# Kernel tuning notes

Measured on AMD Instinct MI355X. Metric: run time of the kernel, lower is better.

The kernel has to match this reference:

```python
import jax, jax.numpy as jnp
import numpy as np

D_MODEL = 384
N_HEADS = 8
HEAD_DIM = D_MODEL // N_HEADS


def setup_inputs() -> dict:
    key = jax.random.key(0)
    ks = jax.random.split(key, 8)
    b, n = 2, 2048
    s = 0.02
    return {
        "x": jax.random.normal(ks[0], (b, n, D_MODEL), jnp.float32),
        "coords": jax.random.normal(ks[1], (b, n, 3), jnp.float32),
        "W_qkv": jax.random.normal(ks[2], (D_MODEL, 3 * D_MODEL), jnp.float32) * s,
        "b_qkv": jnp.zeros((3 * D_MODEL,), jnp.float32),
        "W_dist": jax.random.normal(ks[3], (1, N_HEADS), jnp.float32) * s,
        "b_dist": jnp.zeros((N_HEADS,), jnp.float32),
        "W_out": jax.random.normal(ks[4], (D_MODEL, D_MODEL), jnp.float32) * s,
        "b_out": jnp.zeros((D_MODEL,), jnp.float32),
    }


def reference(x, coords, W_qkv, b_qkv, W_dist, b_dist, W_out, b_out):
    b, n, _ = x.shape
    qkv = x @ W_qkv + b_qkv                       # (b, n, 3*d)
    q, k, v = jnp.split(qkv, 3, axis=-1)
    def heads(t):
        return t.reshape(b, n, N_HEADS, HEAD_DIM).transpose(0, 2, 1, 3)  # b h n d
    q, k, v = heads(q), heads(k), heads(v)
    attn = jnp.einsum('bhid,bhjd->bhij', q, k) / jnp.sqrt(jnp.float32(HEAD_DIM))
    # distance bias: ||c_i - c_j|| projected to heads (Linear(1, n_heads))
    diff = coords[:, :, None, :] - coords[:, None, :, :]   # (b, i, j, 3)
    dist = jnp.sqrt(jnp.sum(diff * diff, axis=-1))         # (b, i, j)
    dist_bias = dist[..., None] * W_dist[0] + b_dist       # (b, i, j, h)
    attn = attn + dist_bias.transpose(0, 3, 1, 2)          # (b, h, i, j)
    attn = jax.nn.softmax(attn, axis=-1)
    out = jnp.einsum('bhij,bhjd->bhid', attn, v)
    out = out.transpose(0, 2, 1, 3).reshape(b, n, D_MODEL)
    return out @ W_out + b_out
```

## Files before the change

### kernel.cpp

```cpp
#include <hip/hip_runtime.h>
#include <hip/hip_bf16.h>

#define NB 2
#define SEQ 2048
#define DM 384
#define NH 8
#define HD 48
#define QKVN 1152

typedef __hip_bfloat16 bf16;
typedef __attribute__((ext_vector_type(8))) short short8;
typedef __attribute__((ext_vector_type(4))) float float4v;
typedef __attribute__((ext_vector_type(16))) float f32x16;

static __device__ __forceinline__ float bf2f(bf16 v){ return __bfloat162float(v); }
static __device__ __forceinline__ float ldin(const void* p, size_t i, int isf){
    return isf ? ((const float*)p)[i] : bf2f(((const bf16*)p)[i]);
}
static __device__ __forceinline__ short f2b(float f){
    union { float f; unsigned u; } a; a.f = f;
    unsigned r = a.u + 0x7FFFu + ((a.u >> 16) & 1u);
    return (short)(r >> 16);
}
static __device__ __forceinline__ unsigned pk2(float a, float b){
    union { __hip_bfloat162 h; unsigned u; } r;
    r.h = __float22bfloat162_rn(float2{a, b});
    return r.u;
}
static __device__ __forceinline__ float bflo(unsigned u){
    union { unsigned u; float f; } a; a.u = u << 16; return a.f;
}
static __device__ __forceinline__ float bfhi(unsigned u){
    union { unsigned u; float f; } a; a.u = u & 0xFFFF0000u; return a.f;
}
static __device__ __forceinline__ short8 u4pack(unsigned w0, unsigned w1, unsigned w2, unsigned w3){
    union { unsigned u[4]; short8 s; } r; r.u[0]=w0; r.u[1]=w1; r.u[2]=w2; r.u[3]=w3; return r.s;
}
static __device__ __forceinline__ int detect_isf(const void* x){
    const unsigned short* xb = (const unsigned short*)x;
    int l = threadIdx.x & 63;
    union { unsigned u; float f; } a; a.u = ((unsigned)xb[2*l]) << 16;
    float ab = fabsf(a.f);
    int good = (a.f == 0.0f) || (ab > 9.765625e-4f && ab < 1024.0f);
    unsigned long long m = __ballot(good);
    return (__popcll(m) >= 32) ? 0 : 1;
}

__global__ __launch_bounds__(256) void k_wt(const void* __restrict__ x,
    const void* __restrict__ Wqkv, short* __restrict__ WqT)
{
    const int isf = detect_isf(x);
    const int t = threadIdx.x;
    const int b = blockIdx.x;
    const int kt = b / 36, nt = b % 36;
    const int k0 = kt*32, n0 = nt*32;
    __shared__ float Ls[32][33];
    for (int idx = t; idx < 1024; idx += 256) {
        int r = idx >> 5, c = idx & 31;
        Ls[r][c] = ldin(Wqkv, (size_t)(k0+r)*QKVN + n0 + c, isf);
    }
    __syncthreads();
    for (int idx = t; idx < 1024; idx += 256) {
        int r2 = idx >> 5, c2 = idx & 31;
        WqT[(size_t)(n0+r2)*DM + k0 + c2] = f2b(Ls[c2][r2]);
    }
}

__global__ __launch_bounds__(256) void k_qkv_dist(const void* __restrict__ x,
    const void* __restrict__ coords,
    const short* __restrict__ WT, const void* __restrict__ bqkv,
    const void* __restrict__ Wout,
    short* __restrict__ qg3, short* __restrict__ kg3, short* __restrict__ vg3,
    short* __restrict__ dist8, short* __restrict__ WoT)
{
    __shared__ __align__(16) short As[64*72];
    __shared__ __align__(16) short Bs[128*72];
    __shared__ float cjx[16], cjy[16], cjz[16];
    const int isf = detect_isf(x);
    const int t = threadIdx.x;
    const int bid = blockIdx.x;
    if (bid >= 1088) {
        const int b = bid - 1088;
        const int kt = b / 12, nt = b % 12;
        const int k0 = kt*32, n0 = nt*32;
        float (*Ls)[33] = (float(*)[33])As;
        for (int idx = t; idx < 1024; idx += 256) {
            int r = idx >> 5, c = idx & 31;
            Ls[r][c] = ldin(Wout, (size_t)(k0+r)*DM + n0 + c, isf);
        }
        __syncthreads();
        for (int idx = t; idx < 1024; idx += 256) {
            int r2 = idx >> 5, c2 = idx & 31;
            WoT[(size_t)(n0+r2)*DM + k0 + c2] = f2b(Ls[c2][r2]);
        }
        return;
    }
    if (bid >= 576) {
        const int b = bid - 576;
        const int bb = b >> 8;
        const int jg = (b >> 1) & 127;
        const int j0 = jg * 16;
        const int ih = (b & 1) * 1024;
        if (t < 16) {
            int gj = (bb*SEQ + j0 + t)*3;
            cjx[t] = ldin(coords, gj, isf);
            cjy[t] = ldin(coords, gj+1, isf);
            cjz[t] = ldin(coords, gj+2, isf);
        }
        __syncthreads();
        #pragma unroll
        for (int k = 0; k < 4; ++k) {
            int i = ih + k*256 + t;
            int gi = (bb*SEQ + i)*3;
            float px = ldin(coords, gi, isf), py = ldin(coords, gi+1, isf), pz = ldin(coords, gi+2, isf);
            short o[16];
            #pragma unroll
            for (int e = 0; e < 16; ++e) {
                float dx = px - cjx[e], dy = py - cjy[e], dz = pz - cjz[e];
                o[e] = f2b(sqrtf(dx*dx + dy*dy + dz*dz));
            }
            short* dst = dist8 + (((size_t)bb*512 + (size_t)jg*4)*SEQ + i)*4;
            *(int2*)(dst)          = *(const int2*)(o);
            *(int2*)(dst + SEQ*4)  = *(const int2*)(o + 4);
            *(int2*)(dst + SEQ*8)  = *(const int2*)(o + 8);
            *(int2*)(dst + SEQ*12) = *(const int2*)(o + 12);
        }
        return;
    }
    const int w = t >> 6, lane = t & 63, L = lane & 15, quad = lane >> 4;
    const int mt = bid / 9, nt = bid % 9;
    const int row0 = mt*64, col0 = nt*128;
    const int wm = w & 1, wn = w >> 1;
    float4v acc[2][4] = {};
    int4 rA[4], rB[4];
    {
        const int k0 = 0;
        #pragma unroll
        for (int ci = 0; ci < 2; ++ci) {
            int c = t + ci*256; int row = c >> 3, k8 = c & 7;
            size_t src = (size_t)(row0+row)*DM + k0 + k8*8;
            if (isf) {
                rA[2*ci]   = *(const int4*)((const float*)x + src);
                rA[2*ci+1] = *(const int4*)((const float*)x + src + 4);
            } else {
                rA[ci] = *(const int4*)((const short*)x + src);
            }
        }
        #pragma unroll
        for (int ci = 0; ci < 4; ++ci) {
            int c = t + ci*256; int row = c >> 3, k8 = c & 7;
            rB[ci] = *(const int4*)(WT + (size_t)(col0+row)*DM + k0 + k8*8);
        }
    }
    for (int ks = 0; ks < 6; ++ks) {
        __syncthreads();
        #pragma unroll
        for (int ci = 0; ci < 2; ++ci) {
            int c = t + ci*256; int row = c >> 3, k8 = c & 7;
            if (isf) {
                union { int4 i[2]; float f[8]; } u; u.i[0] = rA[2*ci]; u.i[1] = rA[2*ci+1];
                short o[8];
                #pragma unroll
                for (int e = 0; e < 8; ++e) o[e] = f2b(u.f[e]);
                *(int4*)(&As[row*72 + k8*8]) = *(const int4*)o;
            } else {
                *(int4*)(&As[row*72 + k8*8]) = rA[ci];
            }
        }
        #pragma unroll
        for (int ci = 0; ci < 4; ++ci) {
            int c = t + ci*256; int row = c >> 3, k8 = c & 7;
            *(int4*)(&Bs[row*72 + k8*8]) = rB[ci];
        }
        __syncthreads();
        if (ks < 5) {
            const int k0 = (ks+1)*64;
            #pragma unroll
            for (int ci = 0; ci < 2; ++ci) {
                int c = t + ci*256; int row = c >> 3, k8 = c & 7;
                size_t src = (size_t)(row0+row)*DM + k0 + k8*8;
                if (isf) {
                    rA[2*ci]   = *(const int4*)((const float*)x + src);
                    rA[2*ci+1] = *(const int4*)((const float*)x + src + 4);
                } else {
                    rA[ci] = *(const int4*)((const short*)x + src);
                }
            }
            #pragma unroll
            for (int ci = 0; ci < 4; ++ci) {
                int c = t + ci*256; int row = c >> 3, k8 = c & 7;
                rB[ci] = *(const int4*)(WT + (size_t)(col0+row)*DM + k0 + k8*8);
            }
        }
        #pragma unroll
        for (int kc = 0; kc < 2; ++kc) {
            short8 a0 = *(const short8*)(&As[(32*wm + L)*72 + kc*32 + quad*8]);
            short8 a1 = *(const short8*)(&As[(32*wm + 16 + L)*72 + kc*32 + quad*8]);
            #pragma unroll
            for (int ni = 0; ni < 4; ++ni) {
                short8 bf = *(const short8*)(&Bs[(64*wn + 16*ni + L)*72 + kc*32 + quad*8]);
                acc[0][ni] = __builtin_amdgcn_mfma_f32_16x16x32_bf16(a0, bf, acc[0][ni], 0, 0, 0);
                acc[1][ni] = __builtin_amdgcn_mfma_f32_16x16x32_bf16(a1, bf, acc[1][ni], 0, 0, 0);
            }
        }
    }
    const int which = col0 / DM;
    const int cbase = col0 % DM;
    short* Ep = Bs;
    __syncthreads();
    if (which < 2) {
        #pragma unroll
        for (int mi = 0; mi < 2; ++mi)
            #pragma unroll
            for (int ni = 0; ni < 4; ++ni) {
                int col_l = 64*wn + 16*ni + L;
                float bv = ldin(bqkv, col0 + col_l, isf);
                #pragma unroll
                for (int r = 0; r < 4; ++r) {
                    int row_l = 32*wm + 16*mi + quad*4 + r;
                    Ep[row_l*136 + col_l] = f2b(acc[mi][ni][r] + bv);
                }
            }
        __syncthreads();
        short* dst = which ? kg3 : qg3;
        for (int c = t; c < 1024; c += 256) {
            int row_l = c >> 4, col_l = (c & 15)*8;
            int row_g = row0 + row_l;
            int bi = row_g >> 11, nn = row_g & (SEQ-1);
            int c2 = cbase + col_l;
            int hh = c2/HD, dh = c2%HD;
            int bh = bi*NH + hh;
            int dc = dh >> 4, hi = (dh >> 3) & 1;
            size_t dstoff = ((size_t)bh*64 + (nn>>5))*1536 + (size_t)((dc*2 + hi)*256 + (nn&31)*8);
            *(int4*)(dst + dstoff) = *(const int4*)(&Ep[row_l*136 + col_l]);
        }
    } else {
        #pragma unroll
        for (int mi = 0; mi < 2; ++mi)
            #pragma unroll
            for (int ni = 0; ni < 4; ++ni) {
                int col_l = 64*wn + 16*ni + L;
                float bv = ldin(bqkv, col0 + col_l, isf);
                #pragma unroll
                for (int r = 0; r < 4; ++r) {
                    int row_l = 32*wm + 16*mi + quad*4 + r;
                    Ep[col_l*72 + row_l] = f2b(acc[mi][ni][r] + bv);
                }
            }
        __syncthreads();
        for (int c = t; c < 1024; c += 256) {
            int col_l = c >> 3, row8 = (c & 7)*8;
            int row_g = row0 + row8;
            int bi = row_g >> 11, nn = row_g & (SEQ-1);
            int c2 = cbase + col_l;
            int hh = c2/HD, dh = c2%HD;
            int bh = bi*NH + hh;
            int jt = nn >> 5, jc = (nn >> 4) & 1;
            int ehalf = ((nn >> 3) & 1)*4;
            int dt = dh >> 5, dp = dh & 31;
            int hstride = dt ? 128 : 256;
            size_t base = ((size_t)bh*64 + jt)*1536 + (size_t)(jc*768 + dt*512 + dp*8 + ehalf);
            *(int2*)(vg3 + base)           = *(const int2*)(&Ep[col_l*72 + row8]);
            *(int2*)(vg3 + base + hstride) = *(const int2*)(&Ep[col_l*72 + row8 + 4]);
        }
    }
}

__global__ __launch_bounds__(256, 4) void k_attn(
    const short* __restrict__ qg3, const short* __restrict__ kg3, const short* __restrict__ vg3,
    const short* __restrict__ dist8, const void* __restrict__ Wdist,
    const void* __restrict__ bdist, short* __restrict__ aob, const void* __restrict__ x)
{
    __shared__ float Ored[2][32*48];
    __shared__ float Lred[2][32];
    const int isf = detect_isf(x);
    const int t = threadIdx.x;
    const int w = t >> 6, lane = t & 63;
    const int li = lane & 31, hi = lane >> 5;
    const int xcd  = blockIdx.x & 7;
    const int slot = blockIdx.x >> 3;
    const int bi   = xcd >> 2;
    const int band = xcd & 3;
    const int hh   = slot & 7;
    const int it   = band*16 + (slot >> 3);
    const int bh   = bi*NH + hh;
    const int i0 = it*32;
    const float log2e = 1.4426950408889634f;
    const float scale2 = 0.14433756729740643f * log2e;
    const float wd = ldin(Wdist, hh, isf) * log2e;
    const float bd = ldin(bdist, hh, isf) * log2e;

    const short* qB = qg3 + ((size_t)bh*64 + it)*1536 + hi*256 + li*8;
    const short8 qf0 = *(const short8*)(qB);
    const short8 qf1 = *(const short8*)(qB + 512);
    const short8 qf2 = *(const short8*)(qB + 1024);

    f32x16 accO0 = {}, accO1 = {};
    float rsum = 0.0f;

    const short* kBp = kg3 + ((size_t)bh*64 + w)*1536 + hi*256 + li*8;
    const short* vBp = vg3 + ((size_t)bh*64 + w)*1536 + li*8;
    const short* dBp = dist8 + (((size_t)bi*512 + (size_t)w*8 + hi)*SEQ + i0 + li)*4;

    for (int s = 0; s < 16; ++s) {
        short8 kf0 = *(const short8*)(kBp);
        short8 kf1 = *(const short8*)(kBp + 512);
        short8 kf2 = *(const short8*)(kBp + 1024);
        int2 du0 = *(const int2*)(dBp);
        int2 du1 = *(const int2*)(dBp + SEQ*8);
        int2 du2 = *(const int2*)(dBp + SEQ*16);
        int2 du3 = *(const int2*)(dBp + SEQ*24);
        f32x16 sacc = {};
        __builtin_amdgcn_s_setprio(1);
        sacc = __builtin_amdgcn_mfma_f32_32x32x16_bf16(kf0, qf0, sacc, 0, 0, 0);
        sacc = __builtin_amdgcn_mfma_f32_32x32x16_bf16(kf1, qf1, sacc, 0, 0, 0);
        sacc = __builtin_amdgcn_mfma_f32_32x32x16_bf16(kf2, qf2, sacc, 0, 0, 0);
        __builtin_amdgcn_s_setprio(0);
        float p[16];
        #pragma unroll
        for (int rq = 0; rq < 4; ++rq) {
            int2 du = rq == 0 ? du0 : rq == 1 ? du1 : rq == 2 ? du2 : du3;
            float d0 = bflo((unsigned)du.x), d1 = bfhi((unsigned)du.x);
            float d2 = bflo((unsigned)du.y), d3 = bfhi((unsigned)du.y);
            p[4*rq+0] = __builtin_amdgcn_exp2f(fmaf(sacc[4*rq+0], scale2, fmaf(d0, wd, bd)));
            p[4*rq+1] = __builtin_amdgcn_exp2f(fmaf(sacc[4*rq+1], scale2, fmaf(d1, wd, bd)));
            p[4*rq+2] = __builtin_amdgcn_exp2f(fmaf(sacc[4*rq+2], scale2, fmaf(d2, wd, bd)));
            p[4*rq+3] = __builtin_amdgcn_exp2f(fmaf(sacc[4*rq+3], scale2, fmaf(d3, wd, bd)));
            rsum += (p[4*rq+0] + p[4*rq+1]) + (p[4*rq+2] + p[4*rq+3]);
        }
        short8 pa0 = u4pack(pk2(p[0],p[1]),  pk2(p[2],p[3]),  pk2(p[4],p[5]),   pk2(p[6],p[7]));
        short8 pa1 = u4pack(pk2(p[8],p[9]),  pk2(p[10],p[11]),pk2(p[12],p[13]), pk2(p[14],p[15]));
        short8 v00 = *(const short8*)(vBp + hi*256);
        short8 v10 = *(const short8*)(vBp + 768 + hi*256);
        short8 v01 = *(const short8*)(vBp + 512 + hi*128);
        short8 v11 = *(const short8*)(vBp + 1280 + hi*128);
        __builtin_amdgcn_s_setprio(1);
        accO0 = __builtin_amdgcn_mfma_f32_32x32x16_bf16(pa0, v00, accO0, 0, 0, 0);
        accO0 = __builtin_amdgcn_mfma_f32_32x32x16_bf16(pa1, v10, accO0, 0, 0, 0);
        accO1 = __builtin_amdgcn_mfma_f32_32x32x16_bf16(pa0, v01, accO1, 0, 0, 0);
        accO1 = __builtin_amdgcn_mfma_f32_32x32x16_bf16(pa1, v11, accO1, 0, 0, 0);
        __builtin_amdgcn_s_setprio(0);
        kBp += 4*1536; vBp += 4*1536; dBp += (size_t)SEQ*128;
    }
    rsum += __shfl_xor(rsum, 32);

    if (w >= 2) {
        float* Od = Ored[w-2];
        #pragma unroll
        for (int r = 0; r < 16; ++r) {
            int ii = (r & 3) + 8*(r >> 2) + 4*hi;
            Od[ii*48 + li] = accO0[r];
            if (li < 16) Od[ii*48 + 32 + li] = accO1[r];
        }
        if (lane < 32) Lred[w-2][lane] = rsum;
    }
    __syncthreads();
    if (w < 2) {
        const float* Od = Ored[w];
        #pragma unroll
        for (int r = 0; r < 16; ++r) {
            int ii = (r & 3) + 8*(r >> 2) + 4*hi;
            accO0[r] += Od[ii*48 + li];
            accO1[r] += Od[ii*48 + 32 + (li & 15)];
        }
        rsum += Lred[w][li];
    }
    __syncthreads();
    if (w == 1) {
        float* Od = Ored[0];
        #pragma unroll
        for (int r = 0; r < 16; ++r) {
            int ii = (r & 3) + 8*(r >> 2) + 4*hi;
            Od[ii*48 + li] = accO0[r];
            if (li < 16) Od[ii*48 + 32 + li] = accO1[r];
        }
        if (lane < 32) Lred[0][lane] = rsum;
    }
    __syncthreads();
    if (w == 0) {
        float* Od = Ored[0];
        #pragma unroll
        for (int r = 0; r < 16; ++r) {
            int ii = (r & 3) + 8*(r >> 2) + 4*hi;
            Od[ii*48 + li] += accO0[r];
            if (li < 16) Od[ii*48 + 32 + li] += accO1[r];
        }
        if (lane < 32) Lred[0][lane] += rsum;
    }
    __syncthreads();
    for (int c = t; c < 192; c += 256) {
        int r = c / 6, d8 = (c % 6)*8;
        float inv = 1.0f / Lred[0][r];
        const float* src = &Ored[0][r*48 + d8];
        short o[8];
        #pragma unroll
        for (int e = 0; e < 8; ++e) o[e] = f2b(src[e]*inv);
        *(int4*)(aob + ((size_t)(bi*SEQ) + i0 + r)*DM + hh*HD + d8) = *(const int4*)o;
    }
}

__global__ __launch_bounds__(256) void k_out(const short* __restrict__ aob,
    const short* __restrict__ WT, const void* __restrict__ bout,
    void* __restrict__ out, const void* __restrict__ x)
{
    __shared__ __align__(16) short As[64*72];
    __shared__ __align__(16) short Bs[128*72];
    const int isf = detect_isf(x);
    const int t = threadIdx.x;
    const int w = t >> 6, lane = t & 63, L = lane & 15, quad = lane >> 4;
    const int mt = blockIdx.x / 3, nt = blockIdx.x % 3;
    const int row0 = mt*64, col0 = nt*128;
    const int wm = w & 1, wn = w >> 1;
    float4v acc[2][4] = {};
    int4 rA[2], rB[4];
    {
        #pragma unroll
        for (int ci = 0; ci < 2; ++ci) {
            int c = t + ci*256; int row = c >> 3, k8 = c & 7;
            rA[ci] = *(const int4*)(aob + (size_t)(row0+row)*DM + k8*8);
        }
        #pragma unroll
        for (int ci = 0; ci < 4; ++ci) {
            int c = t + ci*256; int row = c >> 3, k8 = c & 7;
            rB[ci] = *(const int4*)(WT + (size_t)(col0+row)*DM + k8*8);
        }
    }
    for (int ks = 0; ks < 6; ++ks) {
        __syncthreads();
        #pragma unroll
        for (int ci = 0; ci < 2; ++ci) {
            int c = t + ci*256; int row = c >> 3, k8 = c & 7;
            *(int4*)(&As[row*72 + k8*8]) = rA[ci];
        }
        #pragma unroll
        for (int ci = 0; ci < 4; ++ci) {
            int c = t + ci*256; int row = c >> 3, k8 = c & 7;
            *(int4*)(&Bs[row*72 + k8*8]) = rB[ci];
        }
        __syncthreads();
        if (ks < 5) {
            const int k0 = (ks+1)*64;
            #pragma unroll
            for (int ci = 0; ci < 2; ++ci) {
                int c = t + ci*256; int row = c >> 3, k8 = c & 7;
                rA[ci] = *(const int4*)(aob + (size_t)(row0+row)*DM + k0 + k8*8);
            }
            #pragma unroll
            for (int ci = 0; ci < 4; ++ci) {
                int c = t + ci*256; int row = c >> 3, k8 = c & 7;
                rB[ci] = *(const int4*)(WT + (size_t)(col0+row)*DM + k0 + k8*8);
            }
        }
        #pragma unroll
        for (int kc = 0; kc < 2; ++kc) {
            short8 a0 = *(const short8*)(&As[(32*wm + L)*72 + kc*32 + quad*8]);
            short8 a1 = *(const short8*)(&As[(32*wm + 16 + L)*72 + kc*32 + quad*8]);
            #pragma unroll
            for (int ni = 0; ni < 4; ++ni) {
                short8 bf = *(const short8*)(&Bs[(64*wn + 16*ni + L)*72 + kc*32 + quad*8]);
                acc[0][ni] = __builtin_amdgcn_mfma_f32_16x16x32_bf16(a0, bf, acc[0][ni], 0, 0, 0);
                acc[1][ni] = __builtin_amdgcn_mfma_f32_16x16x32_bf16(a1, bf, acc[1][ni], 0, 0, 0);
            }
        }
    }
    #pragma unroll
    for (int mi = 0; mi < 2; ++mi) {
        #pragma unroll
        for (int ni = 0; ni < 4; ++ni) {
            int col_g = col0 + 64*wn + 16*ni + L;
            float bv = ldin(bout, col_g, isf);
            #pragma unroll
            for (int r = 0; r < 4; ++r) {
                int row_g = row0 + 32*wm + 16*mi + quad*4 + r;
                size_t oi = (size_t)row_g*DM + col_g;
                float val = acc[mi][ni][r] + bv;
                if (isf) ((float*)out)[oi] = val;
                else     ((bf16*)out)[oi]  = __float2bfloat16(val);
            }
        }
    }
}

extern "C" void kernel_launch(void* const* d_in, const int* in_sizes, int n_in,
                              void* d_out, int out_size, void* d_ws, size_t ws_size,
                              hipStream_t stream) {
    const void* x      = d_in[0];
    const void* coords = d_in[1];
    const void* Wqkv   = d_in[2];
    const void* bqkv   = d_in[3];
    const void* Wdist  = d_in[4];
    const void* bdist  = d_in[5];
    const void* Wout   = d_in[6];
    const void* bout   = d_in[7];

    short* qg3   = (short*)d_ws;
    short* kg3   = qg3  + (size_t)1572864;
    short* vg3   = kg3  + (size_t)1572864;
    short* dist8 = vg3  + (size_t)1573120;
    short* aob   = dist8 + (size_t)8388608;
    short* WqT   = aob  + (size_t)1572864;
    short* WoT   = WqT  + (size_t)442368;

    k_wt<<<dim3(432), dim3(256), 0, stream>>>(x, Wqkv, WqT);
    k_qkv_dist<<<dim3(1232), dim3(256), 0, stream>>>(x, coords, WqT, bqkv, Wout,
                                                     qg3, kg3, vg3, dist8, WoT);
    k_attn<<<dim3(1024), dim3(256), 0, stream>>>(qg3, kg3, vg3, dist8, Wdist, bdist, aob, x);
    k_out<<<dim3(192), dim3(256), 0, stream>>>(aob, WoT, bout, d_out, x);
}
```

Before: 160.5 us.

## Load GEMM MFMA fragments directly from global memory, drop LDS staging

The QKV projection and output projection GEMMs no longer stage tiles through shared memory with double-buffered register prefetch and barriers. Each wave now loads its A and B MFMA fragments straight from global memory (converting fp32 inputs to bf16 on the fly). The output GEMM is retiled to 16x64 per wave with twice as many blocks. This removes LDS traffic and __syncthreads, but it relies on L1/L2 for the reuse that shared memory used to provide, and the fragment loads are strided per row, so they may be less coalesced.

```diff
diff --git a/kernel.cpp b/kernel.cpp
--- a/kernel.cpp
+++ b/kernel.cpp
@@ -44,6 +44,17 @@
     int good = (a.f == 0.0f) || (ab > 9.765625e-4f && ab < 1024.0f);
     unsigned long long m = __ballot(good);
     return (__popcll(m) >= 32) ? 0 : 1;
+}
+static __device__ __forceinline__ short8 ldfragA(const void* x, size_t row, int k, int isf){
+    size_t off = row*DM + k;
+    if (isf) {
+        const float* xf = (const float*)x + off;
+        short o[8];
+        #pragma unroll
+        for (int e = 0; e < 8; ++e) o[e] = f2b(xf[e]);
+        return *(const short8*)o;
+    }
+    return *(const short8*)((const short*)x + off);
 }
 
 __global__ __launch_bounds__(256) void k_wt(const void* __restrict__ x,
@@ -73,8 +84,7 @@
     short* __restrict__ qg3, short* __restrict__ kg3, short* __restrict__ vg3,
     short* __restrict__ dist8, short* __restrict__ WoT)
 {
-    __shared__ __align__(16) short As[64*72];
-    __shared__ __align__(16) short Bs[128*72];
+    __shared__ __align__(16) short Ep[128*72];
     __shared__ float cjx[16], cjy[16], cjz[16];
     const int isf = detect_isf(x);
     const int t = threadIdx.x;
@@ -83,7 +93,7 @@
         const int b = bid - 1088;
         const int kt = b / 12, nt = b % 12;
         const int k0 = kt*32, n0 = nt*32;
-        float (*Ls)[33] = (float(*)[33])As;
+        float (*Ls)[33] = (float(*)[33])Ep;
         for (int idx = t; idx < 1024; idx += 256) {
             int r = idx >> 5, c = idx & 31;
             Ls[r][c] = ldin(Wout, (size_t)(k0+r)*DM + n0 + c, isf);
@@ -132,82 +142,23 @@
     const int row0 = mt*64, col0 = nt*128;
     const int wm = w & 1, wn = w >> 1;
     float4v acc[2][4] = {};
-    int4 rA[4], rB[4];
-    {
-        const int k0 = 0;
-        #pragma unroll
-        for (int ci = 0; ci < 2; ++ci) {
-            int c = t + ci*256; int row = c >> 3, k8 = c & 7;
-            size_t src = (size_t)(row0+row)*DM + k0 + k8*8;
-            if (isf) {
-                rA[2*ci]   = *(const int4*)((const float*)x + src);
-                rA[2*ci+1] = *(const int4*)((const float*)x + src + 4);
-            } else {
-                rA[ci] = *(const int4*)((const short*)x + src);
-            }
-        }
-        #pragma unroll
-        for (int ci = 0; ci < 4; ++ci) {
-            int c = t + ci*256; int row = c >> 3, k8 = c & 7;
-            rB[ci] = *(const int4*)(WT + (size_t)(col0+row)*DM + k0 + k8*8);
-        }
-    }
-    for (int ks = 0; ks < 6; ++ks) {
-        __syncthreads();
-        #pragma unroll
-        for (int ci = 0; ci < 2; ++ci) {
-            int c = t + ci*256; int row = c >> 3, k8 = c & 7;
-            if (isf) {
-                union { int4 i[2]; float f[8]; } u; u.i[0] = rA[2*ci]; u.i[1] = rA[2*ci+1];
-                short o[8];
-                #pragma unroll
-                for (int e = 0; e < 8; ++e) o[e] = f2b(u.f[e]);
-                *(int4*)(&As[row*72 + k8*8]) = *(const int4*)o;
-            } else {
-                *(int4*)(&As[row*72 + k8*8]) = rA[ci];
-            }
-        }
-        #pragma unroll
-        for (int ci = 0; ci < 4; ++ci) {
-            int c = t + ci*256; int row = c >> 3, k8 = c & 7;
-            *(int4*)(&Bs[row*72 + k8*8]) = rB[ci];
-        }
-        __syncthreads();
-        if (ks < 5) {
-            const int k0 = (ks+1)*64;
-            #pragma unroll
-            for (int ci = 0; ci < 2; ++ci) {
-                int c = t + ci*256; int row = c >> 3, k8 = c & 7;
-                size_t src = (size_t)(row0+row)*DM + k0 + k8*8;
-                if (isf) {
-                    rA[2*ci]   = *(const int4*)((const float*)x + src);
-                    rA[2*ci+1] = *(const int4*)((const float*)x + src + 4);
-                } else {
-                    rA[ci] = *(const int4*)((const short*)x + src);
-                }
-            }
-            #pragma unroll
-            for (int ci = 0; ci < 4; ++ci) {
-                int c = t + ci*256; int row = c >> 3, k8 = c & 7;
-                rB[ci] = *(const int4*)(WT + (size_t)(col0+row)*DM + k0 + k8*8);
-            }
-        }
-        #pragma unroll
-        for (int kc = 0; kc < 2; ++kc) {
-            short8 a0 = *(const short8*)(&As[(32*wm + L)*72 + kc*32 + quad*8]);
-            short8 a1 = *(const short8*)(&As[(32*wm + 16 + L)*72 + kc*32 + quad*8]);
-            #pragma unroll
-            for (int ni = 0; ni < 4; ++ni) {
-                short8 bf = *(const short8*)(&Bs[(64*wn + 16*ni + L)*72 + kc*32 + quad*8]);
-                acc[0][ni] = __builtin_amdgcn_mfma_f32_16x16x32_bf16(a0, bf, acc[0][ni], 0, 0, 0);
-                acc[1][ni] = __builtin_amdgcn_mfma_f32_16x16x32_bf16(a1, bf, acc[1][ni], 0, 0, 0);
-            }
+    const size_t rA0 = (size_t)(row0 + 32*wm + L);
+    const size_t rA1 = rA0 + 16;
+    const short* wB = WT + (size_t)(col0 + 64*wn + L)*DM;
+    #pragma unroll 4
+    for (int kk = 0; kk < 12; ++kk) {
+        const int k0 = kk*32 + quad*8;
+        short8 a0 = ldfragA(x, rA0, k0, isf);
+        short8 a1 = ldfragA(x, rA1, k0, isf);
+        #pragma unroll
+        for (int ni = 0; ni < 4; ++ni) {
+            short8 bf = *(const short8*)(wB + (size_t)(16*ni)*DM + k0);
+            acc[0][ni] = __builtin_amdgcn_mfma_f32_16x16x32_bf16(a0, bf, acc[0][ni], 0, 0, 0);
+            acc[1][ni] = __builtin_amdgcn_mfma_f32_16x16x32_bf16(a1, bf, acc[1][ni], 0, 0, 0);
         }
     }
     const int which = col0 / DM;
     const int cbase = col0 % DM;
-    short* Ep = Bs;
-    __syncthreads();
     if (which < 2) {
         #pragma unroll
         for (int mi = 0; mi < 2; ++mi)
@@ -403,80 +354,36 @@
     const short* __restrict__ WT, const void* __restrict__ bout,
     void* __restrict__ out, const void* __restrict__ x)
 {
-    __shared__ __align__(16) short As[64*72];
-    __shared__ __align__(16) short Bs[128*72];
     const int isf = detect_isf(x);
     const int t = threadIdx.x;
     const int w = t >> 6, lane = t & 63, L = lane & 15, quad = lane >> 4;
-    const int mt = blockIdx.x / 3, nt = blockIdx.x % 3;
-    const int row0 = mt*64, col0 = nt*128;
-    const int wm = w & 1, wn = w >> 1;
-    float4v acc[2][4] = {};
-    int4 rA[2], rB[4];
-    {
-        #pragma unroll
-        for (int ci = 0; ci < 2; ++ci) {
-            int c = t + ci*256; int row = c >> 3, k8 = c & 7;
-            rA[ci] = *(const int4*)(aob + (size_t)(row0+row)*DM + k8*8);
-        }
-        #pragma unroll
-        for (int ci = 0; ci < 4; ++ci) {
-            int c = t + ci*256; int row = c >> 3, k8 = c & 7;
-            rB[ci] = *(const int4*)(WT + (size_t)(col0+row)*DM + k8*8);
-        }
-    }
-    for (int ks = 0; ks < 6; ++ks) {
-        __syncthreads();
-        #pragma unroll
-        for (int ci = 0; ci < 2; ++ci) {
-            int c = t + ci*256; int row = c >> 3, k8 = c & 7;
-            *(int4*)(&As[row*72 + k8*8]) = rA[ci];
-        }
-        #pragma unroll
-        for (int ci = 0; ci < 4; ++ci) {
-            int c = t + ci*256; int row = c >> 3, k8 = c & 7;
-            *(int4*)(&Bs[row*72 + k8*8]) = rB[ci];
-        }
-        __syncthreads();
-        if (ks < 5) {
-            const int k0 = (ks+1)*64;
-            #pragma unroll
-            for (int ci = 0; ci < 2; ++ci) {
-                int c = t + ci*256; int row = c >> 3, k8 = c & 7;
-                rA[ci] = *(const int4*)(aob + (size_t)(row0+row)*DM + k0 + k8*8);
-            }
-            #pragma unroll
-            for (int ci = 0; ci < 4; ++ci) {
-                int c = t + ci*256; int row = c >> 3, k8 = c & 7;
-                rB[ci] = *(const int4*)(WT + (size_t)(col0+row)*DM + k0 + k8*8);
-            }
-        }
-        #pragma unroll
-        for (int kc = 0; kc < 2; ++kc) {
-            short8 a0 = *(const short8*)(&As[(32*wm + L)*72 + kc*32 + quad*8]);
-            short8 a1 = *(const short8*)(&As[(32*wm + 16 + L)*72 + kc*32 + quad*8]);
-            #pragma unroll
-            for (int ni = 0; ni < 4; ++ni) {
-                short8 bf = *(const short8*)(&Bs[(64*wn + 16*ni + L)*72 + kc*32 + quad*8]);
-                acc[0][ni] = __builtin_amdgcn_mfma_f32_16x16x32_bf16(a0, bf, acc[0][ni], 0, 0, 0);
-                acc[1][ni] = __builtin_amdgcn_mfma_f32_16x16x32_bf16(a1, bf, acc[1][ni], 0, 0, 0);
-            }
+    const int mt = (blockIdx.x / 6)*4 + w;
+    const int nt = blockIdx.x % 6;
+    const int row0 = mt*16, col0 = nt*64;
+    float4v acc[4] = {};
+    const short* aB = aob + (size_t)(row0 + L)*DM;
+    const short* wB = WT + (size_t)(col0 + L)*DM;
+    #pragma unroll 4
+    for (int kk = 0; kk < 12; ++kk) {
+        const int k0 = kk*32 + quad*8;
+        short8 a0 = *(const short8*)(aB + k0);
+        #pragma unroll
+        for (int ni = 0; ni < 4; ++ni) {
+            short8 bf = *(const short8*)(wB + (size_t)(16*ni)*DM + k0);
+            acc[ni] = __builtin_amdgcn_mfma_f32_16x16x32_bf16(a0, bf, acc[ni], 0, 0, 0);
         }
     }
     #pragma unroll
-    for (int mi = 0; mi < 2; ++mi) {
-        #pragma unroll
-        for (int ni = 0; ni < 4; ++ni) {
-            int col_g = col0 + 64*wn + 16*ni + L;
-            float bv = ldin(bout, col_g, isf);
-            #pragma unroll
-            for (int r = 0; r < 4; ++r) {
-                int row_g = row0 + 32*wm + 16*mi + quad*4 + r;
-                size_t oi = (size_t)row_g*DM + col_g;
-                float val = acc[mi][ni][r] + bv;
-                if (isf) ((float*)out)[oi] = val;
-                else     ((bf16*)out)[oi]  = __float2bfloat16(val);
-            }
+    for (int ni = 0; ni < 4; ++ni) {
+        int col_g = col0 + 16*ni + L;
+        float bv = ldin(bout, col_g, isf);
+        #pragma unroll
+        for (int r = 0; r < 4; ++r) {
+            int row_g = row0 + quad*4 + r;
+            size_t oi = (size_t)row_g*DM + col_g;
+            float val = acc[ni][r] + bv;
+            if (isf) ((float*)out)[oi] = val;
+            else     ((bf16*)out)[oi]  = __float2bfloat16(val);
         }
     }
 }
@@ -505,5 +412,5 @@
     k_qkv_dist<<<dim3(1232), dim3(256), 0, stream>>>(x, coords, WqT, bqkv, Wout,
                                                      qg3, kg3, vg3, dist8, WoT);
     k_attn<<<dim3(1024), dim3(256), 0, stream>>>(qg3, kg3, vg3, dist8, Wdist, bdist, aob, x);
-    k_out<<<dim3(192), dim3(256), 0, stream>>>(aob, WoT, bout, d_out, x);
-}
+    k_out<<<dim3(384), dim3(256), 0, stream>>>(aob, WoT, bout, d_out, x);
+}
```

After: 156.6 us. -2.4%, faster.
